# Optimization experiments

Measured on AMD Instinct MI355X. Metric: run time of the kernel, lower is better.

The kernel has to match this reference:

```python
import jax, jax.numpy as jnp
import numpy as np

B, NUM_IN = 256, 4096
C1, C2 = 64, 128
K1, K2, P1, P2 = 9, 5, 4, 2
POOL1, POOL2 = 4, 4
H = 256            # rnn_hidden_size
H1, H2 = 256, 128  # mlp hidden sizes
EPS = 1e-5


def setup_inputs() -> dict:
    key = jax.random.key(0)
    ks = jax.random.split(key, 24)
    g = lambda k, shp, scale=0.02: (jax.random.normal(k, shp, jnp.float32) * scale)
    return {
        "x": jax.random.normal(ks[0], (B, 1, NUM_IN), jnp.float32),
        "s": jax.random.normal(ks[1], (B, 1), jnp.float32),
        "conv1_w": g(ks[2], (C1, 1, K1), 0.1), "conv1_b": g(ks[3], (C1,)),
        "bn1_g": jnp.ones((C1,), jnp.float32), "bn1_b": jnp.zeros((C1,), jnp.float32),
        "conv2_w": g(ks[4], (C2, C1, K2), 0.05), "conv2_b": g(ks[5], (C2,)),
        "bn2_g": jnp.ones((C2,), jnp.float32), "bn2_b": jnp.zeros((C2,), jnp.float32),
        "lstm_wi0": g(ks[6], (C2, 4 * H), 0.05), "lstm_bi0": g(ks[7], (4 * H,)),
        "lstm_wh0": g(ks[8], (H, 4 * H), 0.05), "lstm_bh0": g(ks[9], (4 * H,)),
        "lstm_wi1": g(ks[10], (H, 4 * H), 0.05), "lstm_bi1": g(ks[11], (4 * H,)),
        "lstm_wh1": g(ks[12], (H, 4 * H), 0.05), "lstm_bh1": g(ks[13], (4 * H,)),
        "w1": g(ks[14], (H + 1, H1), 0.05), "b1": g(ks[15], (H1,)),
        "w2": g(ks[16], (H1, H2), 0.05), "b2": g(ks[17], (H2,)),
        "wp": g(ks[18], (H2, 1), 0.05), "bp": g(ks[19], (1,)),
    }


def _conv1d(x, w, b, stride, pad):
    # x: [B,C,L], w: [O,I,K]
    y = jax.lax.conv_general_dilated(x, w, (stride,), [(pad, pad)],
                                     dimension_numbers=("NCH", "OIH", "NCH"))
    return y + b[None, :, None]


def _avgpool(x, k):
    Bx, Cx, L = x.shape
    return x.reshape(Bx, Cx, L // k, k).mean(axis=-1)


def _bn(x, gamma, beta):
    # training-mode batchnorm over (N, L) per channel, biased variance
    mu = x.mean(axis=(0, 2), keepdims=True)
    var = ((x - mu) ** 2).mean(axis=(0, 2), keepdims=True)
    xh = (x - mu) * jax.lax.rsqrt(var + EPS)
    return xh * gamma[None, :, None] + beta[None, :, None]


def _lstm_cell(xt, h, c, wi, bi, wh, bh):
    gates = xt @ wi + bi + h @ wh + bh
    i, f, g, o = jnp.split(gates, 4, axis=-1)
    c_new = jax.nn.sigmoid(f) * c + jax.nn.sigmoid(i) * jnp.tanh(g)
    h_new = jax.nn.sigmoid(o) * jnp.tanh(c_new)
    return h_new, c_new


def reference(x, s, conv1_w, conv1_b, bn1_g, bn1_b, conv2_w, conv2_b, bn2_g, bn2_b,
              lstm_wi0, lstm_bi0, lstm_wh0, lstm_bh0,
              lstm_wi1, lstm_bi1, lstm_wh1, lstm_bh1,
              w1, b1, w2, b2, wp, bp):
    x = _bn(_avgpool(jax.nn.relu(_conv1d(x, conv1_w, conv1_b, 1, P1)), POOL1), bn1_g, bn1_b)
    x = _bn(_avgpool(jax.nn.relu(_conv1d(x, conv2_w, conv2_b, 1, P2)), POOL2), bn2_g, bn2_b)
    seq = jnp.transpose(x, (0, 2, 1))          # [B, T, C2]
    seq_t = jnp.transpose(seq, (1, 0, 2))      # [T, B, C2]
    Bx = seq.shape[0]
    init = (jnp.zeros((Bx, H), x.dtype), jnp.zeros((Bx, H), x.dtype),
            jnp.zeros((Bx, H), x.dtype), jnp.zeros((Bx, H), x.dtype))

    def step(carry, xt):
        h0, c0, h1, c1 = carry
        h0, c0 = _lstm_cell(xt, h0, c0, lstm_wi0, lstm_bi0, lstm_wh0, lstm_bh0)
        h1, c1 = _lstm_cell(h0, h1, c1, lstm_wi1, lstm_bi1, lstm_wh1, lstm_bh1)
        return (h0, c0, h1, c1), None

    (h0, c0, h1, c1), _ = jax.lax.scan(step, init, seq_t)
    feat = jnp.concatenate([h1, s], axis=1)    # [B, H+1]
    z = jax.nn.relu(feat @ w1 + b1)            # dropout is identity at eval
    z = jax.nn.relu(z @ w2 + b2)
    return jax.nn.softplus(z @ wp + bp)        # [B, 1]
```

## Files before the change

### kernel.cpp

```cpp
#include <hip/hip_runtime.h>
#include <hip/hip_bf16.h>
#include <hip/hip_fp16.h>
#include <math.h>

#define EPSV 1e-5f

typedef short short8 __attribute__((ext_vector_type(8)));
typedef float f32x4 __attribute__((ext_vector_type(4)));
typedef unsigned long long u64;

#define MFMA(a, b, c) __builtin_amdgcn_mfma_f32_16x16x32_f16(a, b, c, 0, 0, 0)

#define OFF_SC1    8192
#define OFF_SH1    8448
#define OFF_SC2    8704
#define OFF_SH2    9216
#define OFF_B0     9728
#define OFF_B1     13824
#define OFF_PART1  17920
#define OFF_PART2  148992
#define OFF_W2F    411136
#define OFF_WF     493056
#define OFF_SEQ    2328064
#define OFF_H0W    19105280
#define OFF_H1W    19629568
#define OFF_HF     20153856

__device__ __forceinline__ unsigned short f2h(float f) {
  return __half_as_ushort(__float2half(f));
}
__device__ __forceinline__ float h2f(unsigned short u) {
  return __half2float(__ushort_as_half(u));
}
__device__ __forceinline__ float sigf(float x) { return 1.f / (1.f + __expf(-x)); }
__device__ __forceinline__ float tanhfast(float x) {
  return 1.f - 2.f / (__expf(2.f * x) + 1.f);
}

__global__ void k_init(u64* hz) {
  hz[blockIdx.x * 256 + threadIdx.x] = 0ULL;
}

__global__ __launch_bounds__(256, 2) void k_conv1(const float* __restrict__ x,
                                                  const float* __restrict__ w1,
                                                  const float* __restrict__ b1,
                                                  float* __restrict__ part1) {
  __shared__ float xs[4104];
  __shared__ float w1s[576];
  __shared__ float b1s[64];
  __shared__ float red[64][4][2];
  const int tid = threadIdx.x, b = blockIdx.x;
  for (int j = tid; j < 4104; j += 256) {
    int p = j - 4;
    xs[j] = (p >= 0 && p < 4096) ? x[b * 4096 + p] : 0.f;
  }
  for (int j = tid; j < 576; j += 256) w1s[j] = w1[j];
  if (tid < 64) b1s[tid] = b1[tid];
  __syncthreads();
  const int c = tid >> 2, lq = tid & 3;
  float wr[9];
#pragma unroll
  for (int k = 0; k < 9; k++) wr[k] = w1s[c * 9 + k];
  const float bb = b1s[c];
  float S = 0.f, SS = 0.f;
  for (int li = 0; li < 256; li++) {
    int l = lq * 256 + li;
    int base = 4 * l;
    float a4 = 0.f;
#pragma unroll
    for (int jj = 0; jj < 4; jj++) {
      float cv = bb;
#pragma unroll
      for (int k = 0; k < 9; k++) cv += xs[base + jj + k] * wr[k];
      a4 += fmaxf(cv, 0.f);
    }
    float y = 0.25f * a4;
    S += y;
    SS += y * y;
  }
  red[c][lq][0] = S;
  red[c][lq][1] = SS;
  __syncthreads();
  if (tid < 64) {
    float s = 0.f, ss = 0.f;
#pragma unroll
    for (int q = 0; q < 4; q++) {
      s += red[tid][q][0];
      ss += red[tid][q][1];
    }
    part1[(b * 64 + tid) * 2 + 0] = s;
    part1[(b * 64 + tid) * 2 + 1] = ss;
  }
}

__global__ void k_bn1(const float* __restrict__ part1, const float* __restrict__ g,
                      const float* __restrict__ bt, float* __restrict__ sc,
                      float* __restrict__ sh) {
  __shared__ float rs[256], rss[256];
  const int c = blockIdx.x, tid = threadIdx.x;
  rs[tid] = part1[(tid * 64 + c) * 2 + 0];
  rss[tid] = part1[(tid * 64 + c) * 2 + 1];
  __syncthreads();
  for (int st = 128; st > 0; st >>= 1) {
    if (tid < st) {
      rs[tid] += rs[tid + st];
      rss[tid] += rss[tid + st];
    }
    __syncthreads();
  }
  if (tid == 0) {
    const float N = 256.f * 1024.f;
    float mean = rs[0] / N;
    float var = rss[0] / N - mean * mean;
    float scale = g[c] * rsqrtf(var + EPSV);
    sc[c] = scale;
    sh[c] = bt[c] - mean * scale;
  }
}

__global__ void k_w2frag(const float* __restrict__ w2,
                         unsigned short* __restrict__ w2f) {
  int n = blockIdx.x * 256 + threadIdx.x;
  if (n >= 40960) return;
  int e = n & 7, lane = (n >> 3) & 63, ot = (n >> 9) & 7, sc = n >> 12;
  int s = sc >> 1, c2 = sc & 1;
  int o = ot * 16 + (lane & 15);
  int i = c2 * 32 + ((lane >> 4) << 3) + e;
  w2f[n] = f2h(w2[o * 320 + i * 5 + s]);
}

__global__ __launch_bounds__(256, 1) void k_conv2(
    const float* __restrict__ x, const float* __restrict__ w1,
    const float* __restrict__ b1, const float* __restrict__ sc1,
    const float* __restrict__ sh1, const unsigned short* __restrict__ w2f,
    const float* __restrict__ b2, unsigned short* __restrict__ seq,
    float* __restrict__ part2) {
  __shared__ float xs[4104];
  __shared__ unsigned short y1t[1028][66];
  __shared__ float w1s[576], b1s[64], s1s[64], h1s[64], b2s[128];
  __shared__ float red[4][2][128];
  const int tid = threadIdx.x, b = blockIdx.x;
  for (int j = tid; j < 4104; j += 256) {
    int p = j - 4;
    xs[j] = (p >= 0 && p < 4096) ? x[b * 4096 + p] : 0.f;
  }
  for (int j = tid; j < 576; j += 256) w1s[j] = w1[j];
  if (tid < 64) {
    b1s[tid] = b1[tid];
    s1s[tid] = sc1[tid];
    h1s[tid] = sh1[tid];
  }
  if (tid < 128) b2s[tid] = b2[tid];
  if (tid < 132) {
    int r4 = tid / 33, c4 = tid % 33;
    int row = (r4 < 2) ? r4 : (1024 + r4);
    ((unsigned int*)&y1t[row][0])[c4] = 0u;
  }
  __syncthreads();
  {
    const int i2 = tid & 31, lg = tid >> 5;
    const int ia = 2 * i2, ib = ia + 1;
    float wra[9], wrb[9];
#pragma unroll
    for (int k = 0; k < 9; k++) {
      wra[k] = w1s[ia * 9 + k];
      wrb[k] = w1s[ib * 9 + k];
    }
    const float bia = b1s[ia], bib = b1s[ib];
    const float sa = s1s[ia], sb = s1s[ib], ha = h1s[ia], hb = h1s[ib];
    for (int j = 0; j < 128; j++) {
      int l = lg * 128 + j;
      float xv[12];
#pragma unroll
      for (int m = 0; m < 12; m++) xv[m] = xs[4 * l + m];
      float aa = 0.f, ab = 0.f;
#pragma unroll
      for (int jj = 0; jj < 4; jj++) {
        float ca = bia, cb = bib;
#pragma unroll
        for (int k = 0; k < 9; k++) {
          float xx = xv[jj + k];
          ca += xx * wra[k];
          cb += xx * wrb[k];
        }
        aa += fmaxf(ca, 0.f);
        ab += fmaxf(cb, 0.f);
      }
      float va = 0.25f * aa * sa + ha;
      float vb = 0.25f * ab * sb + hb;
      unsigned int pk = (unsigned int)f2h(va) | ((unsigned int)f2h(vb) << 16);
      *(unsigned int*)&y1t[l + 2][ia] = pk;
    }
  }
  __syncthreads();
  const int wv = tid >> 6, lane = tid & 63;
  const int colo = lane & 15, rq = lane >> 4;
  float Sa[2][4], SSa[2][4];
#pragma unroll
  for (int a = 0; a < 2; a++)
#pragma unroll
    for (int c = 0; c < 4; c++) {
      Sa[a][c] = 0.f;
      SSa[a][c] = 0.f;
    }
#pragma unroll
  for (int og = 0; og < 2; og++) {
    short8 bf[4][10];
#pragma unroll
    for (int ot = 0; ot < 4; ot++)
#pragma unroll
      for (int sc = 0; sc < 10; sc++)
        bf[ot][sc] = *(const short8*)(w2f + ((sc * 8 + og * 4 + ot) * 64 + lane) * 8);
    for (int ltw = 0; ltw < 16; ltw++) {
      int lt = wv * 16 + ltw;
      int lbase = lt * 16;
      short8 af[10];
#pragma unroll
      for (int s = 0; s < 5; s++)
#pragma unroll
        for (int c2 = 0; c2 < 2; c2++)
          af[s * 2 + c2] =
              *(const short8*)&y1t[lbase + colo + s][c2 * 32 + rq * 8];
#pragma unroll
      for (int ot = 0; ot < 4; ot++) {
        f32x4 acc = {0.f, 0.f, 0.f, 0.f};
#pragma unroll
        for (int sc = 0; sc < 10; sc++)
          acc = MFMA(af[sc], bf[ot][sc], acc);
        int o = (og * 4 + ot) * 16 + colo;
        float bv = b2s[o];
        float s4 = fmaxf(acc[0] + bv, 0.f) + fmaxf(acc[1] + bv, 0.f) +
                   fmaxf(acc[2] + bv, 0.f) + fmaxf(acc[3] + bv, 0.f);
        float y = 0.25f * s4;
        int t_out = lt * 4 + rq;
        seq[(b * 256 + t_out) * 128 + o] = f2h(y);
        Sa[og][ot] += y;
        SSa[og][ot] += y * y;
      }
    }
  }
#pragma unroll
  for (int og = 0; og < 2; og++)
#pragma unroll
    for (int ot = 0; ot < 4; ot++) {
      float sv = Sa[og][ot], ssv = SSa[og][ot];
      sv += __shfl_xor(sv, 16, 64);
      sv += __shfl_xor(sv, 32, 64);
      ssv += __shfl_xor(ssv, 16, 64);
      ssv += __shfl_xor(ssv, 32, 64);
      if (rq == 0) {
        int o = (og * 4 + ot) * 16 + colo;
        red[wv][0][o] = sv;
        red[wv][1][o] = ssv;
      }
    }
  __syncthreads();
  if (tid < 128) {
    float s = red[0][0][tid] + red[1][0][tid] + red[2][0][tid] + red[3][0][tid];
    float ss = red[0][1][tid] + red[1][1][tid] + red[2][1][tid] + red[3][1][tid];
    part2[(b * 128 + tid) * 2 + 0] = s;
    part2[(b * 128 + tid) * 2 + 1] = ss;
  }
}

__global__ void k_bn2(const float* __restrict__ part2, const float* __restrict__ g,
                      const float* __restrict__ bt, float* __restrict__ sc,
                      float* __restrict__ sh) {
  __shared__ float rs[256], rss[256];
  const int o = blockIdx.x, tid = threadIdx.x;
  rs[tid] = part2[(tid * 128 + o) * 2 + 0];
  rss[tid] = part2[(tid * 128 + o) * 2 + 1];
  __syncthreads();
  for (int st = 128; st > 0; st >>= 1) {
    if (tid < st) {
      rs[tid] += rs[tid + st];
      rss[tid] += rss[tid + st];
    }
    __syncthreads();
  }
  if (tid == 0) {
    const float N = 65536.f;
    float mean = rs[0] / N;
    float var = rss[0] / N - mean * mean;
    float scale = g[o] * rsqrtf(var + EPSV);
    sc[o] = scale;
    sh[o] = bt[o] - mean * scale;
  }
}

__global__ void k_bias(const float* __restrict__ bi0, const float* __restrict__ bh0,
                       const float* __restrict__ wi0, const float* __restrict__ sh2,
                       const float* __restrict__ bi1, const float* __restrict__ bh1,
                       float* __restrict__ b0arr, float* __restrict__ b1arr) {
  int g = blockIdx.x * 256 + threadIdx.x;
  float s = bi0[g] + bh0[g];
  for (int k = 0; k < 128; k++) s += sh2[k] * wi0[k * 1024 + g];
  b0arr[g] = s;
  b1arr[g] = bi1[g] + bh1[g];
}

__global__ void k_wfrag(const float* __restrict__ wi0, const float* __restrict__ wh0,
                        const float* __restrict__ wi1, const float* __restrict__ wh1,
                        const float* __restrict__ sc2,
                        unsigned short* __restrict__ wf) {
  const int slot = blockIdx.x / 56;
  const int idx = (blockIdx.x % 56) * 256 + threadIdx.x;
  const int j = idx >> 9, lane = (idx >> 3) & 63, e = idx & 7;
  const int sh = slot >> 2, wv = slot & 3;
  const int m = lane & 15;
  const int gcol = (m & 3) * 256 + sh * 16 + wv * 4 + (m >> 2);
  float v;
  if (j < 12) {
    int k = j * 32 + ((lane >> 4) << 3) + e;
    v = (k < 128) ? sc2[k] * wi0[k * 1024 + gcol] : wh0[(k - 128) * 1024 + gcol];
  } else {
    int k = (j - 12) * 32 + ((lane >> 4) << 3) + e;
    v = (k < 256) ? wi1[k * 1024 + gcol] : wh1[(k - 256) * 1024 + gcol];
  }
  wf[slot * 14336 + idx] = f2h(v);
}

__global__ __launch_bounds__(256, 1) void k_lstm(
    const unsigned short* __restrict__ seq, const unsigned short* __restrict__ wf,
    const float* __restrict__ b0arr, const float* __restrict__ b1arr,
    u64* __restrict__ h0w, u64* __restrict__ h1w, float* __restrict__ hfinal) {
  __shared__ unsigned short wlds[4 * 28 * 64 * 8];
  __shared__ unsigned short hs0[2][16 * 264];
  __shared__ unsigned short hs1[2][16 * 264];
  const int tid = threadIdx.x;
  const int gb = blockIdx.x >> 4, sh = blockIdx.x & 15;
  const int b0 = gb * 16;
  const int wv = tid >> 6, lane = tid & 63;
  const int bt = lane & 15;
  const int ul = lane >> 4;
  const int q8 = ul * 8;

  {
    const u64* src = (const u64*)(wf + sh * 4 * 14336);
    u64* dst = (u64*)wlds;
    for (int j = tid; j < 14336; j += 256) dst[j] = src[j];
  }
#define LW(j) (*(const short8*)&wlds[(((wv)*28 + (j)) * 64 + lane) * 8])

  f32x4 b0v, b1v;
#pragma unroll
  for (int r = 0; r < 4; r++) {
    int gcol = r * 256 + sh * 16 + wv * 4 + ul;
    b0v[r] = b0arr[gcol];
    b1v[r] = b1arr[gcol];
  }
  float c0 = 0.f, c1 = 0.f, h1v = 0.f;
  const int pidx = (sh * 8 + wv * 2 + (ul >> 1)) * 16 + bt;
  u64* const st0base = h0w + gb * 2048 + pidx;
  u64* const st1base = h1w + gb * 2048 + pidx;
  __syncthreads();

  {
    const unsigned short* xp = seq + ((b0 + bt) * 256 + 0) * 128 + q8;
    short8 xa0 = *(const short8*)(xp + 0);
    short8 xa1 = *(const short8*)(xp + 32);
    short8 xa2 = *(const short8*)(xp + 64);
    short8 xa3 = *(const short8*)(xp + 96);
    f32x4 acc = b0v;
    acc = MFMA(LW(0), xa0, acc);
    acc = MFMA(LW(1), xa1, acc);
    acc = MFMA(LW(2), xa2, acc);
    acc = MFMA(LW(3), xa3, acc);
    c0 = sigf(acc[1]) * c0 + sigf(acc[0]) * tanhfast(acc[2]);
    float h0v = sigf(acc[3]) * tanhfast(c0);
    unsigned v0 = f2h(h0v);
    unsigned v1 = __shfl_down(v0, 16, 64);
    if ((ul & 1) == 0) {
      u64 w = 1ULL | ((u64)v0 << 16) | ((u64)v1 << 32);
      __hip_atomic_store(st0base, w, __ATOMIC_RELAXED, __HIP_MEMORY_SCOPE_AGENT);
    }
  }

  for (int t = 0; t < 256; t++) {
    short8 xa0, xa1, xa2, xa3;
    if (t < 255) {
      const unsigned short* xp = seq + ((b0 + bt) * 256 + (t + 1)) * 128 + q8;
      xa0 = *(const short8*)(xp + 0);
      xa1 = *(const short8*)(xp + 32);
      xa2 = *(const short8*)(xp + 64);
      xa3 = *(const short8*)(xp + 96);
    }
    const u64* q0 = h0w + (t & 1) * 32768 + gb * 2048;
    const u64* q1 = h1w + ((t + 1) & 1) * 32768 + gb * 2048;
    const unsigned e0 = (unsigned)(t + 1), e1 = (unsigned)t;
    u64 w0[8], w1[8];
    for (;;) {
      bool ok = true;
#pragma unroll
      for (int u = 0; u < 8; u++) {
        w0[u] = __hip_atomic_load(q0 + u * 256 + tid, __ATOMIC_RELAXED,
                                  __HIP_MEMORY_SCOPE_AGENT);
        w1[u] = __hip_atomic_load(q1 + u * 256 + tid, __ATOMIC_RELAXED,
                                  __HIP_MEMORY_SCOPE_AGENT);
      }
#pragma unroll
      for (int u = 0; u < 8; u++)
        ok = ok & ((unsigned)(unsigned short)w0[u] == e0) &
             ((unsigned)(unsigned short)w1[u] == e1);
      if (__all(ok)) break;
    }
    const int hb = t & 1;
#pragma unroll
    for (int u = 0; u < 8; u++) {
      int g = u * 256 + tid;
      int bw = g & 15, p = g >> 4;
      *(unsigned*)&hs0[hb][bw * 264 + 2 * p] = (unsigned)(w0[u] >> 16);
      *(unsigned*)&hs1[hb][bw * 264 + 2 * p] = (unsigned)(w1[u] >> 16);
    }
    __syncthreads();
    short8 ha[8], hbf[8];
#pragma unroll
    for (int kk = 0; kk < 8; kk++) {
      ha[kk] = *(const short8*)&hs0[hb][bt * 264 + kk * 32 + q8];
      hbf[kk] = *(const short8*)&hs1[hb][bt * 264 + kk * 32 + q8];
    }
    f32x4 acc1a = b1v;
    f32x4 acc1b = {0.f, 0.f, 0.f, 0.f};
#pragma unroll
    for (int kk = 0; kk < 8; kk++) {
      acc1a = MFMA(LW(12 + kk), ha[kk], acc1a);
      acc1b = MFMA(LW(20 + kk), hbf[kk], acc1b);
    }
    f32x4 acc0 = b0v;
    if (t < 255) {
      acc0 = MFMA(LW(0), xa0, acc0);
      acc0 = MFMA(LW(1), xa1, acc0);
      acc0 = MFMA(LW(2), xa2, acc0);
      acc0 = MFMA(LW(3), xa3, acc0);
#pragma unroll
      for (int kk = 0; kk < 8; kk++) acc0 = MFMA(LW(4 + kk), ha[kk], acc0);
    }
    {
      float gi = acc1a[0] + acc1b[0], gf = acc1a[1] + acc1b[1];
      float gg = acc1a[2] + acc1b[2], go = acc1a[3] + acc1b[3];
      c1 = sigf(gf) * c1 + sigf(gi) * tanhfast(gg);
      h1v = sigf(go) * tanhfast(c1);
      unsigned v0 = f2h(h1v);
      unsigned v1 = __shfl_down(v0, 16, 64);
      if ((ul & 1) == 0) {
        u64 w = (u64)(unsigned short)(t + 1) | ((u64)v0 << 16) | ((u64)v1 << 32);
        __hip_atomic_store(st1base + (t & 1) * 32768, w, __ATOMIC_RELAXED,
                           __HIP_MEMORY_SCOPE_AGENT);
      }
    }
    if (t < 255) {
      c0 = sigf(acc0[1]) * c0 + sigf(acc0[0]) * tanhfast(acc0[2]);
      float h0v = sigf(acc0[3]) * tanhfast(c0);
      unsigned v0 = f2h(h0v);
      unsigned v1 = __shfl_down(v0, 16, 64);
      if ((ul & 1) == 0) {
        u64 w = (u64)(unsigned short)(t + 2) | ((u64)v0 << 16) | ((u64)v1 << 32);
        __hip_atomic_store(st0base + ((t + 1) & 1) * 32768, w, __ATOMIC_RELAXED,
                           __HIP_MEMORY_SCOPE_AGENT);
      }
    }
  }
  hfinal[(b0 + bt) * 256 + sh * 16 + wv * 4 + ul] = h1v;
}

__global__ __launch_bounds__(256, 2) void k_mlp(const float* __restrict__ hfinal,
                                                const float* __restrict__ s,
                                                const float* __restrict__ w1,
                                                const float* __restrict__ b1,
                                                const float* __restrict__ w2,
                                                const float* __restrict__ b2,
                                                const float* __restrict__ wp,
                                                const float* __restrict__ bp,
                                                float* __restrict__ out) {
  __shared__ float feat[257];
  __shared__ float z1[256];
  __shared__ float z2[128];
  const int tid = threadIdx.x, b = blockIdx.x;
  feat[tid] = hfinal[b * 256 + tid];
  if (tid == 0) feat[256] = s[b];
  __syncthreads();
  float a = b1[tid];
  for (int i = 0; i < 257; i++) a += feat[i] * w1[i * 256 + tid];
  z1[tid] = fmaxf(a, 0.f);
  __syncthreads();
  if (tid < 128) {
    float a2 = b2[tid];
    for (int i = 0; i < 256; i++) a2 += z1[i] * w2[i * 128 + tid];
    z2[tid] = fmaxf(a2, 0.f);
  }
  __syncthreads();
  if (tid == 0) {
    float sv = bp[0];
    for (int i = 0; i < 128; i++) sv += z2[i] * wp[i];
    out[b] = fmaxf(sv, 0.f) + log1pf(__expf(-fabsf(sv)));
  }
}

extern "C" void kernel_launch(void* const* d_in, const int* in_sizes, int n_in,
                              void* d_out, int out_size, void* d_ws, size_t ws_size,
                              hipStream_t stream) {
  const float* x = (const float*)d_in[0];
  const float* s = (const float*)d_in[1];
  const float* c1w = (const float*)d_in[2];
  const float* c1b = (const float*)d_in[3];
  const float* bn1g = (const float*)d_in[4];
  const float* bn1b = (const float*)d_in[5];
  const float* c2w = (const float*)d_in[6];
  const float* c2b = (const float*)d_in[7];
  const float* bn2g = (const float*)d_in[8];
  const float* bn2b = (const float*)d_in[9];
  const float* wi0 = (const float*)d_in[10];
  const float* bi0 = (const float*)d_in[11];
  const float* wh0 = (const float*)d_in[12];
  const float* bh0 = (const float*)d_in[13];
  const float* wi1 = (const float*)d_in[14];
  const float* bi1 = (const float*)d_in[15];
  const float* wh1 = (const float*)d_in[16];
  const float* bh1 = (const float*)d_in[17];
  const float* w1 = (const float*)d_in[18];
  const float* b1 = (const float*)d_in[19];
  const float* w2 = (const float*)d_in[20];
  const float* b2 = (const float*)d_in[21];
  const float* wp = (const float*)d_in[22];
  const float* bp = (const float*)d_in[23];

  char* ws = (char*)d_ws;
  float* sc1 = (float*)(ws + OFF_SC1);
  float* sh1 = (float*)(ws + OFF_SH1);
  float* sc2 = (float*)(ws + OFF_SC2);
  float* sh2 = (float*)(ws + OFF_SH2);
  float* b0arr = (float*)(ws + OFF_B0);
  float* b1arr = (float*)(ws + OFF_B1);
  float* part1 = (float*)(ws + OFF_PART1);
  float* part2 = (float*)(ws + OFF_PART2);
  unsigned short* w2f = (unsigned short*)(ws + OFF_W2F);
  unsigned short* wf = (unsigned short*)(ws + OFF_WF);
  unsigned short* seq = (unsigned short*)(ws + OFF_SEQ);
  u64* h0w = (u64*)(ws + OFF_H0W);
  u64* h1w = (u64*)(ws + OFF_H1W);
  float* hf = (float*)(ws + OFF_HF);

  k_init<<<512, 256, 0, stream>>>(h0w);
  k_conv1<<<256, 256, 0, stream>>>(x, c1w, c1b, part1);
  k_bn1<<<64, 256, 0, stream>>>(part1, bn1g, bn1b, sc1, sh1);
  k_w2frag<<<160, 256, 0, stream>>>(c2w, w2f);
  k_conv2<<<256, 256, 0, stream>>>(x, c1w, c1b, sc1, sh1, w2f, c2b, seq, part2);
  k_bn2<<<128, 256, 0, stream>>>(part2, bn2g, bn2b, sc2, sh2);
  k_bias<<<4, 256, 0, stream>>>(bi0, bh0, wi0, sh2, bi1, bh1, b0arr, b1arr);
  k_wfrag<<<3584, 256, 0, stream>>>(wi0, wh0, wi1, wh1, sc2, wf);
  k_lstm<<<256, 256, 0, stream>>>(seq, wf, b0arr, b1arr, h0w, h1w, hf);
  k_mlp<<<256, 256, 0, stream>>>(hf, s, w1, b1, w2, b2, wp, bp, (float*)d_out);
}
```

Before: 841.2 us.

## Reorder LSTM wavefront step to publish layer-0 state first and split spin waits

Inside the persistent LSTM loop, the single combined spin on both layers' flags becomes two waits: first on layer-0 h (with s_sleep backoff after a few spins), then on layer-1 h. Layer-0 gates are now computed and published before layer-1, with the MFMA chain split into two accumulators to shorten dependency latency. This puts the critical-path layer-0 state in the hands of other blocks sooner. The final layer-1 store is skipped at the last step. The sleep backoff may add wakeup latency when a flag arrives just after the sleep starts.

```diff
diff --git a/kernel.cpp b/kernel.cpp
--- a/kernel.cpp
+++ b/kernel.cpp
@@ -389,20 +389,39 @@
     const u64* q1 = h1w + ((t + 1) & 1) * 32768 + gb * 2048;
     const unsigned e0 = (unsigned)(t + 1), e1 = (unsigned)t;
     u64 w0[8], w1[8];
-    for (;;) {
+#pragma unroll
+    for (int u = 0; u < 8; u++)
+      w1[u] = __hip_atomic_load(q1 + u * 256 + tid, __ATOMIC_RELAXED,
+                                __HIP_MEMORY_SCOPE_AGENT);
+    {
+      int spin = 0;
+      for (;;) {
+        bool ok = true;
+#pragma unroll
+        for (int u = 0; u < 8; u++)
+          w0[u] = __hip_atomic_load(q0 + u * 256 + tid, __ATOMIC_RELAXED,
+                                    __HIP_MEMORY_SCOPE_AGENT);
+#pragma unroll
+        for (int u = 0; u < 8; u++)
+          ok = ok & ((unsigned)(unsigned short)w0[u] == e0);
+        if (__all(ok)) break;
+        if (++spin > 2) __builtin_amdgcn_s_sleep(2);
+      }
+    }
+    {
       bool ok = true;
 #pragma unroll
-      for (int u = 0; u < 8; u++) {
-        w0[u] = __hip_atomic_load(q0 + u * 256 + tid, __ATOMIC_RELAXED,
-                                  __HIP_MEMORY_SCOPE_AGENT);
-        w1[u] = __hip_atomic_load(q1 + u * 256 + tid, __ATOMIC_RELAXED,
-                                  __HIP_MEMORY_SCOPE_AGENT);
-      }
-#pragma unroll
       for (int u = 0; u < 8; u++)
-        ok = ok & ((unsigned)(unsigned short)w0[u] == e0) &
-             ((unsigned)(unsigned short)w1[u] == e1);
-      if (__all(ok)) break;
+        ok = ok & ((unsigned)(unsigned short)w1[u] == e1);
+      while (!__all(ok)) {
+        ok = true;
+#pragma unroll
+        for (int u = 0; u < 8; u++) {
+          w1[u] = __hip_atomic_load(q1 + u * 256 + tid, __ATOMIC_RELAXED,
+                                    __HIP_MEMORY_SCOPE_AGENT);
+          ok = ok & ((unsigned)(unsigned short)w1[u] == e1);
+        }
+      }
     }
     const int hb = t & 1;
 #pragma unroll
@@ -419,44 +438,50 @@
       ha[kk] = *(const short8*)&hs0[hb][bt * 264 + kk * 32 + q8];
       hbf[kk] = *(const short8*)&hs1[hb][bt * 264 + kk * 32 + q8];
     }
-    f32x4 acc1a = b1v;
-    f32x4 acc1b = {0.f, 0.f, 0.f, 0.f};
-#pragma unroll
-    for (int kk = 0; kk < 8; kk++) {
-      acc1a = MFMA(LW(12 + kk), ha[kk], acc1a);
-      acc1b = MFMA(LW(20 + kk), hbf[kk], acc1b);
-    }
-    f32x4 acc0 = b0v;
     if (t < 255) {
-      acc0 = MFMA(LW(0), xa0, acc0);
-      acc0 = MFMA(LW(1), xa1, acc0);
-      acc0 = MFMA(LW(2), xa2, acc0);
-      acc0 = MFMA(LW(3), xa3, acc0);
-#pragma unroll
-      for (int kk = 0; kk < 8; kk++) acc0 = MFMA(LW(4 + kk), ha[kk], acc0);
-    }
-    {
-      float gi = acc1a[0] + acc1b[0], gf = acc1a[1] + acc1b[1];
-      float gg = acc1a[2] + acc1b[2], go = acc1a[3] + acc1b[3];
-      c1 = sigf(gf) * c1 + sigf(gi) * tanhfast(gg);
-      h1v = sigf(go) * tanhfast(c1);
-      unsigned v0 = f2h(h1v);
-      unsigned v1 = __shfl_down(v0, 16, 64);
-      if ((ul & 1) == 0) {
-        u64 w = (u64)(unsigned short)(t + 1) | ((u64)v0 << 16) | ((u64)v1 << 32);
-        __hip_atomic_store(st1base + (t & 1) * 32768, w, __ATOMIC_RELAXED,
-                           __HIP_MEMORY_SCOPE_AGENT);
-      }
-    }
-    if (t < 255) {
-      c0 = sigf(acc0[1]) * c0 + sigf(acc0[0]) * tanhfast(acc0[2]);
-      float h0v = sigf(acc0[3]) * tanhfast(c0);
+      f32x4 a0a = b0v;
+      f32x4 a0b = {0.f, 0.f, 0.f, 0.f};
+      a0a = MFMA(LW(0), xa0, a0a);
+      a0b = MFMA(LW(1), xa1, a0b);
+      a0a = MFMA(LW(2), xa2, a0a);
+      a0b = MFMA(LW(3), xa3, a0b);
+#pragma unroll
+      for (int kk = 0; kk < 8; kk += 2) {
+        a0a = MFMA(LW(4 + kk), ha[kk], a0a);
+        a0b = MFMA(LW(5 + kk), ha[kk + 1], a0b);
+      }
+      float gi = a0a[0] + a0b[0], gf = a0a[1] + a0b[1];
+      float gg = a0a[2] + a0b[2], go = a0a[3] + a0b[3];
+      c0 = sigf(gf) * c0 + sigf(gi) * tanhfast(gg);
+      float h0v = sigf(go) * tanhfast(c0);
       unsigned v0 = f2h(h0v);
       unsigned v1 = __shfl_down(v0, 16, 64);
       if ((ul & 1) == 0) {
         u64 w = (u64)(unsigned short)(t + 2) | ((u64)v0 << 16) | ((u64)v1 << 32);
         __hip_atomic_store(st0base + ((t + 1) & 1) * 32768, w, __ATOMIC_RELAXED,
                            __HIP_MEMORY_SCOPE_AGENT);
+      }
+    }
+    {
+      f32x4 acc1a = b1v;
+      f32x4 acc1b = {0.f, 0.f, 0.f, 0.f};
+#pragma unroll
+      for (int kk = 0; kk < 8; kk++) {
+        acc1a = MFMA(LW(12 + kk), ha[kk], acc1a);
+        acc1b = MFMA(LW(20 + kk), hbf[kk], acc1b);
+      }
+      float gi = acc1a[0] + acc1b[0], gf = acc1a[1] + acc1b[1];
+      float gg = acc1a[2] + acc1b[2], go = acc1a[3] + acc1b[3];
+      c1 = sigf(gf) * c1 + sigf(gi) * tanhfast(gg);
+      h1v = sigf(go) * tanhfast(c1);
+      if (t < 255) {
+        unsigned v0 = f2h(h1v);
+        unsigned v1 = __shfl_down(v0, 16, 64);
+        if ((ul & 1) == 0) {
+          u64 w = (u64)(unsigned short)(t + 1) | ((u64)v0 << 16) | ((u64)v1 << 32);
+          __hip_atomic_store(st1base + (t & 1) * 32768, w, __ATOMIC_RELAXED,
+                             __HIP_MEMORY_SCOPE_AGENT);
+        }
       }
     }
   }
```

New measurement: 918.1 us. 9.1% more time.

## Spin on sentinel flags, split layer-0 MFMA chain, reorder LSTM publish

Applied to the files above, without the earlier changes.

The persistent LSTM kernel now spins on two sentinel words per thread before doing the full 16-word flag-checked load, which reduces polling traffic on the global handoff buffers. Block indexing is remapped so blocks sharing a batch group are spread across consecutive block IDs. The layer-0 MFMA chain is split into two independent accumulators to shorten the dependency chain. Layer-0 h is computed and published before layer-1 so other blocks waiting on it see it sooner, and the final-step layer-1 store is skipped. The tradeoffs are an extra load round after the spin and a different placement of blocks across CUs.

```diff
diff --git a/kernel.cpp b/kernel.cpp
--- a/kernel.cpp
+++ b/kernel.cpp
@@ -328,7 +328,7 @@
   __shared__ unsigned short hs0[2][16 * 264];
   __shared__ unsigned short hs1[2][16 * 264];
   const int tid = threadIdx.x;
-  const int gb = blockIdx.x >> 4, sh = blockIdx.x & 15;
+  const int gb = blockIdx.x & 15, sh = blockIdx.x >> 4;
   const int b0 = gb * 16;
   const int wv = tid >> 6, lane = tid & 63;
   const int bt = lane & 15;
@@ -387,7 +387,19 @@
     }
     const u64* q0 = h0w + (t & 1) * 32768 + gb * 2048;
     const u64* q1 = h1w + ((t + 1) & 1) * 32768 + gb * 2048;
-    const unsigned e0 = (unsigned)(t + 1), e1 = (unsigned)t;
+    const unsigned e0 = (unsigned)(unsigned short)(t + 1);
+    const unsigned e1 = (unsigned)(unsigned short)t;
+    {
+      const u64* s0p = q0 + tid * 8;
+      const u64* s1p = q1 + tid * 8 + 7;
+      for (;;) {
+        u64 s0 = __hip_atomic_load(s0p, __ATOMIC_RELAXED, __HIP_MEMORY_SCOPE_AGENT);
+        u64 s1 = __hip_atomic_load(s1p, __ATOMIC_RELAXED, __HIP_MEMORY_SCOPE_AGENT);
+        bool ok = ((unsigned)(unsigned short)s0 == e0) &
+                  ((unsigned)(unsigned short)s1 == e1);
+        if (__all(ok)) break;
+      }
+    }
     u64 w0[8], w1[8];
     for (;;) {
       bool ok = true;
@@ -426,37 +438,45 @@
       acc1a = MFMA(LW(12 + kk), ha[kk], acc1a);
       acc1b = MFMA(LW(20 + kk), hbf[kk], acc1b);
     }
-    f32x4 acc0 = b0v;
+    f32x4 acc0a = b0v;
+    f32x4 acc0b = {0.f, 0.f, 0.f, 0.f};
     if (t < 255) {
-      acc0 = MFMA(LW(0), xa0, acc0);
-      acc0 = MFMA(LW(1), xa1, acc0);
-      acc0 = MFMA(LW(2), xa2, acc0);
-      acc0 = MFMA(LW(3), xa3, acc0);
-#pragma unroll
-      for (int kk = 0; kk < 8; kk++) acc0 = MFMA(LW(4 + kk), ha[kk], acc0);
-    }
-    {
-      float gi = acc1a[0] + acc1b[0], gf = acc1a[1] + acc1b[1];
-      float gg = acc1a[2] + acc1b[2], go = acc1a[3] + acc1b[3];
-      c1 = sigf(gf) * c1 + sigf(gi) * tanhfast(gg);
-      h1v = sigf(go) * tanhfast(c1);
-      unsigned v0 = f2h(h1v);
-      unsigned v1 = __shfl_down(v0, 16, 64);
-      if ((ul & 1) == 0) {
-        u64 w = (u64)(unsigned short)(t + 1) | ((u64)v0 << 16) | ((u64)v1 << 32);
-        __hip_atomic_store(st1base + (t & 1) * 32768, w, __ATOMIC_RELAXED,
-                           __HIP_MEMORY_SCOPE_AGENT);
+      acc0a = MFMA(LW(0), xa0, acc0a);
+      acc0b = MFMA(LW(1), xa1, acc0b);
+      acc0a = MFMA(LW(2), xa2, acc0a);
+      acc0b = MFMA(LW(3), xa3, acc0b);
+#pragma unroll
+      for (int kk = 0; kk < 8; kk += 2) {
+        acc0a = MFMA(LW(4 + kk), ha[kk], acc0a);
+        acc0b = MFMA(LW(5 + kk), ha[kk + 1], acc0b);
       }
     }
     if (t < 255) {
-      c0 = sigf(acc0[1]) * c0 + sigf(acc0[0]) * tanhfast(acc0[2]);
-      float h0v = sigf(acc0[3]) * tanhfast(c0);
+      float gi = acc0a[0] + acc0b[0], gf = acc0a[1] + acc0b[1];
+      float gg = acc0a[2] + acc0b[2], go = acc0a[3] + acc0b[3];
+      c0 = sigf(gf) * c0 + sigf(gi) * tanhfast(gg);
+      float h0v = sigf(go) * tanhfast(c0);
       unsigned v0 = f2h(h0v);
       unsigned v1 = __shfl_down(v0, 16, 64);
       if ((ul & 1) == 0) {
         u64 w = (u64)(unsigned short)(t + 2) | ((u64)v0 << 16) | ((u64)v1 << 32);
         __hip_atomic_store(st0base + ((t + 1) & 1) * 32768, w, __ATOMIC_RELAXED,
                            __HIP_MEMORY_SCOPE_AGENT);
+      }
+    }
+    {
+      float gi = acc1a[0] + acc1b[0], gf = acc1a[1] + acc1b[1];
+      float gg = acc1a[2] + acc1b[2], go = acc1a[3] + acc1b[3];
+      c1 = sigf(gf) * c1 + sigf(gi) * tanhfast(gg);
+      h1v = sigf(go) * tanhfast(c1);
+      if (t < 255) {
+        unsigned v0 = f2h(h1v);
+        unsigned v1 = __shfl_down(v0, 16, 64);
+        if ((ul & 1) == 0) {
+          u64 w = (u64)(unsigned short)(t + 1) | ((u64)v0 << 16) | ((u64)v1 << 32);
+          __hip_atomic_store(st1base + (t & 1) * 32768, w, __ATOMIC_RELAXED,
+                             __HIP_MEMORY_SCOPE_AGENT);
+        }
       }
     }
   }
```

Measured after the change: 846.2 us. About the same (+0.6%).
